# Kernel optimization log

Hardware: AMD Instinct MI355X
Metric: run time of the kernel (lower is better)

## Reference

```python
import jax, jax.numpy as jnp
import numpy as np

T, B, IN, H, L = 512, 128, 1024, 1024, 4
SCALE = 0.02  # scale randn-init weights so tanh/sigmoid stay in a sane range


def setup_inputs() -> dict:
    key = jax.random.key(0)
    ks = jax.random.split(key, 12)
    f32 = jnp.float32
    return {
        "x": jax.random.normal(ks[0], (T, B, IN), f32),
        "hidden": jax.random.normal(ks[1], (2 * L, B, H), f32) * 0.1,
        "Wii": jax.random.normal(ks[2], (L, 3 * H, IN), f32) * SCALE,
        "Wic": jax.random.normal(ks[3], (L, 3 * H, H), f32) * SCALE,
        "Wih": jax.random.normal(ks[4], (L, 3 * H, H), f32) * SCALE,
        "bii": jax.random.normal(ks[5], (L, 3 * H), f32) * SCALE,
        "bic": jax.random.normal(ks[6], (L, 3 * H), f32) * SCALE,
        "bih": jax.random.normal(ks[7], (L, 3 * H), f32) * SCALE,
        "Whh": jax.random.normal(ks[8], (L, H, H), f32) * SCALE,
        "bhh": jax.random.normal(ks[9], (L, H), f32) * SCALE,
        "Wir": jax.random.normal(ks[10], (L, H, IN), f32) * SCALE,
    }


def _res_lstm_scan(x, hidden, Wii, Wic, Wih, bii, bic, bih, Whh, bhh, Wir):
    n_layers = Wii.shape[0]
    h0, c0 = jnp.split(hidden, 2, axis=0)  # each [L, B, H]

    def step(carry, xt):
        h, c = carry
        out = xt
        new_h, new_c = [], []
        for j in range(n_layers):
            hj, cj = h[j], c[j]
            gates = (out @ Wii[j].T + bii[j]
                     + hj @ Wih[j].T + bih[j]
                     + cj @ Wic[j].T + bic[j])  # [B, 3H]
            i_g, f_g, o_g = jnp.split(gates, 3, axis=1)
            cellgate = jnp.tanh(hj @ Whh[j].T + bhh[j])
            cy = jax.nn.sigmoid(f_g) * cj + jax.nn.sigmoid(i_g) * cellgate
            hy = jax.nn.sigmoid(o_g) * (jnp.tanh(cy) + out @ Wir[j].T)
            out = hy
            new_h.append(hy)
            new_c.append(cy)
        return (jnp.stack(new_h), jnp.stack(new_c)), out

    (hF, cF), outputs = jax.lax.scan(step, (h0, c0), x)
    return outputs, hF, cF


def reference(x, hidden, Wii, Wic, Wih, bii, bic, bih, Whh, bhh, Wir):
    return _res_lstm_scan(x, hidden, Wii, Wic, Wih, bii, bic, bih, Whh, bhh, Wir)
```

## Files before the change

### kernel.cpp

```cpp
#include <hip/hip_runtime.h>


#define TT 512
#define BB 128
#define IN_D 1024
#define HH 1024
#define LL 4
#define G3 3072
#define NSUPER (TT + LL - 1)
#define KC 64
#define NCHUNK 48
#define SB_TILE 2048
#define SB_BUF 8192
#define SLOT (BB * HH)
#define SLOT_ALL (LL * SLOT)

typedef __attribute__((ext_vector_type(8))) __bf16 bf16x8;
typedef __attribute__((ext_vector_type(4))) __bf16 bf16x4;
typedef __attribute__((ext_vector_type(4))) float f32x4;

typedef __attribute__((address_space(3))) void lds_void;
typedef const __attribute__((address_space(1))) void gmem_void;

__device__ __forceinline__ void gload_lds16(const void* g, void* l) {
    __builtin_amdgcn_global_load_lds((gmem_void*)g, (lds_void*)l, 16, 0, 0);
}

__device__ __forceinline__ f32x4 mfma16(bf16x8 a, bf16x8 b, f32x4 c) {
    return __builtin_amdgcn_mfma_f32_16x16x32_bf16(a, b, c, 0, 0, 0);
}

__device__ __forceinline__ bf16x8 ldb(const __bf16* p, int k) {
    return *reinterpret_cast<const bf16x8*>(p + k);
}

__device__ __forceinline__ bf16x8 load_a(const float* p, int k) {
    float4 a0 = *reinterpret_cast<const float4*>(p + k);
    float4 a1 = *reinterpret_cast<const float4*>(p + k + 4);
    bf16x8 r;
    r[0] = (__bf16)a0.x; r[1] = (__bf16)a0.y; r[2] = (__bf16)a0.z; r[3] = (__bf16)a0.w;
    r[4] = (__bf16)a1.x; r[5] = (__bf16)a1.y; r[6] = (__bf16)a1.z; r[7] = (__bf16)a1.w;
    return r;
}

__device__ __forceinline__ float sigm(float v) { return 1.f / (1.f + __expf(-v)); }
__device__ __forceinline__ float tanh_fast(float v) { return 1.f - 2.f / (1.f + __expf(2.f * v)); }

__global__ void k_conv_gates(const float* __restrict__ Wii,
                             const float* __restrict__ Wic,
                             const float* __restrict__ Wih,
                             __bf16* __restrict__ Wg) {
    const unsigned total = (unsigned)LL * G3 * G3;
    const unsigned stride = gridDim.x * blockDim.x * 4u;
    for (unsigned idx = (blockIdx.x * blockDim.x + threadIdx.x) * 4u; idx < total; idx += stride) {
        unsigned row = idx / G3;
        int k = (int)(idx - row * G3);
        const float* src; int ks;
        if (k < 1024)      { src = Wii; ks = k; }
        else if (k < 2048) { src = Wih; ks = k - 1024; }
        else               { src = Wic; ks = k - 2048; }
        float4 v = *reinterpret_cast<const float4*>(src + (size_t)row * 1024 + ks);
        bf16x4 o;
        o[0] = (__bf16)v.x; o[1] = (__bf16)v.y; o[2] = (__bf16)v.z; o[3] = (__bf16)v.w;
        *reinterpret_cast<bf16x4*>(Wg + idx) = o;
    }
}

__global__ void k_conv_plain(const float* __restrict__ s, __bf16* __restrict__ d, unsigned total) {
    const unsigned stride = gridDim.x * blockDim.x * 4u;
    for (unsigned idx = (blockIdx.x * blockDim.x + threadIdx.x) * 4u; idx < total; idx += stride) {
        float4 v = *reinterpret_cast<const float4*>(s + idx);
        bf16x4 o;
        o[0] = (__bf16)v.x; o[1] = (__bf16)v.y; o[2] = (__bf16)v.z; o[3] = (__bf16)v.w;
        *reinterpret_cast<bf16x4*>(d + idx) = o;
    }
}

__global__ void k_bias(const float* __restrict__ bii, const float* __restrict__ bic,
                       const float* __restrict__ bih, const float* __restrict__ bhh,
                       float* __restrict__ bsum) {
    int i = blockIdx.x * blockDim.x + threadIdx.x;
    int j = i >> 12, n = i & 4095;
    if (j >= LL) return;
    if (n < G3) bsum[j * 4096 + n] = bii[j * G3 + n] + bih[j * G3 + n] + bic[j * G3 + n];
    else        bsum[j * 4096 + n] = bhh[j * HH + (n - G3)];
}

__global__ void k_init(const float* __restrict__ hidden,
                       float* __restrict__ cbufF, __bf16* __restrict__ hb, __bf16* __restrict__ cb) {
    const unsigned stride = gridDim.x * blockDim.x;
    for (unsigned i = blockIdx.x * blockDim.x + threadIdx.x; i < SLOT_ALL; i += stride) {
        float hv = hidden[i];
        float cv = hidden[SLOT_ALL + i];
        hb[SLOT_ALL + i] = (__bf16)hv;
        cb[SLOT_ALL + i] = (__bf16)cv;
        cbufF[SLOT_ALL + i] = cv;
    }
}

__global__ void k_final(const float* __restrict__ hfin, const float* __restrict__ cbufF,
                        float* __restrict__ out_tail) {
    const unsigned stride = gridDim.x * blockDim.x;
    for (unsigned i = blockIdx.x * blockDim.x + threadIdx.x; i < SLOT_ALL; i += stride) {
        out_tail[i] = hfin[i];
        out_tail[SLOT_ALL + i] = cbufF[SLOT_ALL + i];
    }
}

__global__ __launch_bounds__(512) void k_super(
    const float* __restrict__ x,
    const __bf16* __restrict__ Wg,
    const __bf16* __restrict__ Whh,
    const __bf16* __restrict__ Wir,
    const float* __restrict__ bsum,
    float* __restrict__ cbufF,
    __bf16* __restrict__ hb,
    __bf16* __restrict__ cb,
    float* __restrict__ hfin,
    float* __restrict__ dout,
    int s)
{
    const int j = blockIdx.y;
    const int t = s - j;
    if (t < 0 || t >= TT) return;

    __shared__ __align__(16) char smem[3 * SB_BUF];

    const int p = t & 1, pp = p ^ 1;
    const float*  csrcF = cbufF + (size_t)pp * SLOT_ALL + (size_t)j * SLOT;
    float*        cdstF = cbufF + (size_t)p  * SLOT_ALL + (size_t)j * SLOT;
    const __bf16* hsrcB = hb + (size_t)pp * SLOT_ALL + (size_t)j * SLOT;
    const __bf16* csrcB = cb + (size_t)pp * SLOT_ALL + (size_t)j * SLOT;
    const __bf16* osrcB = hb + (size_t)p * SLOT_ALL + (size_t)(j - 1) * SLOT;
    const float*  osrcF = x + (size_t)t * SLOT;
    __bf16* hdstB = hb + (size_t)p * SLOT_ALL + (size_t)j * SLOT;
    __bf16* cdstB = cb + (size_t)p * SLOT_ALL + (size_t)j * SLOT;

    const int tid  = threadIdx.x;
    const int lane = tid & 63;
    const int wave = tid >> 6;
    const int lrow = lane & 15;
    const int kgrp = lane >> 4;
    const int n0 = blockIdx.x * 16;
    const int m0 = wave * 16;

    const int st_tile = wave >> 1;
    const int st_half = wave & 1;
    const int st_r = st_half * 8 + (lane >> 3);
    const int st_s = lane & 7;
    const int st_k8 = ((st_s ^ (st_r & 7)) << 3);
    const __bf16* Wgj = Wg + (size_t)j * G3 * G3;
    const __bf16* st_g  = Wgj + (size_t)(st_tile * 1024 + n0 + st_r) * G3 + st_k8;
    const __bf16* st_wr = Wir + (size_t)j * HH * IN_D + (size_t)(n0 + st_r) * IN_D + st_k8;
    const __bf16* st_wc = Whh + (size_t)j * HH * HH + (size_t)(n0 + st_r) * HH + st_k8;
    char* st_dst = smem + st_tile * SB_TILE + st_half * 1024;

    auto stage = [&](int c) {
        if (c >= NCHUNK) return;
        char* dst = st_dst + (c % 3) * SB_BUF;
        if (st_tile < 3) {
            gload_lds16(st_g + (size_t)c * KC, dst);
        } else {
            const int r = c >> 4, kb = (c & 15) << 6;
            if (r == 0)      gload_lds16(st_wr + kb, dst);
            else if (r == 1) gload_lds16(st_wc + kb, dst);
        }
    };

    const int dsrow = lrow << 7;
    const int x7 = lrow & 7;
    const int so0 = ((kgrp ^ x7) << 4);
    const int so1 = (((4 | kgrp) ^ x7) << 4);

    const int aoff = (m0 + lrow) * HH + (kgrp << 3);
    const __bf16* aH = hsrcB + aoff;
    const __bf16* aC = csrcB + aoff;
    const __bf16* aO = osrcB + aoff;
    const float*  aX = osrcF + aoff;

    auto loadA = [&](int c, bf16x8& r0, bf16x8& r1) {
        const int rg = c >> 4, kt = (c & 15) << 6;
        if (rg == 0) {
            if (j == 0) { r0 = load_a(aX, kt); r1 = load_a(aX, kt + 32); }
            else        { r0 = ldb(aO, kt);    r1 = ldb(aO, kt + 32); }
        } else if (rg == 1) { r0 = ldb(aH, kt); r1 = ldb(aH, kt + 32); }
        else                { r0 = ldb(aC, kt); r1 = ldb(aC, kt + 32); }
    };

    f32x4 vi = {0,0,0,0}, vf = {0,0,0,0}, vo = {0,0,0,0}, vc = {0,0,0,0}, vr = {0,0,0,0};

    bf16x8 a0, a1, na0, na1;
    stage(0); stage(1);
    loadA(0, a0, a1);
    asm volatile("s_waitcnt vmcnt(3)" ::: "memory");
    __builtin_amdgcn_s_barrier();

    for (int c = 0; c < NCHUNK; ++c) {
        const int rg = c >> 4;
        char* bs = smem + (c % 3) * SB_BUF;

        if (c + 1 < NCHUNK) loadA(c + 1, na0, na1);
        stage(c + 2);

        bf16x8 b;
        b = *(const bf16x8*)(bs + 0 * SB_TILE + dsrow + so0); vi = mfma16(a0, b, vi);
        b = *(const bf16x8*)(bs + 1 * SB_TILE + dsrow + so0); vf = mfma16(a0, b, vf);
        b = *(const bf16x8*)(bs + 2 * SB_TILE + dsrow + so0); vo = mfma16(a0, b, vo);
        if (rg == 0)      { b = *(const bf16x8*)(bs + 3 * SB_TILE + dsrow + so0); vr = mfma16(a0, b, vr); }
        else if (rg == 1) { b = *(const bf16x8*)(bs + 3 * SB_TILE + dsrow + so0); vc = mfma16(a0, b, vc); }
        b = *(const bf16x8*)(bs + 0 * SB_TILE + dsrow + so1); vi = mfma16(a1, b, vi);
        b = *(const bf16x8*)(bs + 1 * SB_TILE + dsrow + so1); vf = mfma16(a1, b, vf);
        b = *(const bf16x8*)(bs + 2 * SB_TILE + dsrow + so1); vo = mfma16(a1, b, vo);
        if (rg == 0)      { b = *(const bf16x8*)(bs + 3 * SB_TILE + dsrow + so1); vr = mfma16(a1, b, vr); }
        else if (rg == 1) { b = *(const bf16x8*)(bs + 3 * SB_TILE + dsrow + so1); vc = mfma16(a1, b, vc); }

        a0 = na0; a1 = na1;
        asm volatile("s_waitcnt vmcnt(3)" ::: "memory");
        __builtin_amdgcn_s_barrier();
    }

    const int col = n0 + lrow;
    const float b_i = bsum[j * 4096 + col];
    const float b_f = bsum[j * 4096 + HH + col];
    const float b_o = bsum[j * 4096 + 2 * HH + col];
    const float b_c = bsum[j * 4096 + G3 + col];

    #pragma unroll
    for (int r = 0; r < 4; ++r) {
        const int m = m0 + kgrp * 4 + r;
        const size_t o = (size_t)m * HH + col;
        float iv = vi[r] + b_i;
        float fv = vf[r] + b_f;
        float ov = vo[r] + b_o;
        float cg = tanh_fast(vc[r] + b_c);
        float cold = csrcF[o];
        float cy = sigm(fv) * cold + sigm(iv) * cg;
        float hy = sigm(ov) * (tanh_fast(cy) + vr[r]);
        cdstF[o] = cy;
        cdstB[o] = (__bf16)cy;
        hdstB[o] = (__bf16)hy;
        if (t == TT - 1) hfin[(size_t)j * SLOT + o] = hy;
        if (j == LL - 1) dout[(size_t)t * SLOT + o] = hy;
    }
}

extern "C" void kernel_launch(void* const* d_in, const int* in_sizes, int n_in,
                              void* d_out, int out_size, void* d_ws, size_t ws_size,
                              hipStream_t stream) {
    const float* x      = (const float*)d_in[0];
    const float* hidden = (const float*)d_in[1];
    const float* Wii    = (const float*)d_in[2];
    const float* Wic    = (const float*)d_in[3];
    const float* Wih    = (const float*)d_in[4];
    const float* bii    = (const float*)d_in[5];
    const float* bic    = (const float*)d_in[6];
    const float* bih    = (const float*)d_in[7];
    const float* Whh    = (const float*)d_in[8];
    const float* bhh    = (const float*)d_in[9];
    const float* Wir    = (const float*)d_in[10];
    float* out = (float*)d_out;

    char* ws = (char*)d_ws;
    __bf16* Wg    = (__bf16*)(ws);
    __bf16* Whh_b = (__bf16*)(ws + 75497472);
    __bf16* Wir_b = (__bf16*)(ws + 83886080);
    float*  cbufF = (float*)(ws + 92274688);
    float*  bsum  = (float*)(ws + 96468992);
    __bf16* hb    = (__bf16*)(ws + 96534528);
    __bf16* cb    = (__bf16*)(ws + 98631680);
    float*  hfin  = (float*)(ws + 100728832);

    k_conv_gates<<<4096, 256, 0, stream>>>(Wii, Wic, Wih, Wg);
    k_conv_plain<<<2048, 256, 0, stream>>>(Whh, Whh_b, (unsigned)(LL * HH * HH));
    k_conv_plain<<<2048, 256, 0, stream>>>(Wir, Wir_b, (unsigned)(LL * HH * IN_D));
    k_bias<<<64, 256, 0, stream>>>(bii, bic, bih, bhh, bsum);
    k_init<<<1024, 256, 0, stream>>>(hidden, cbufF, hb, cb);

    dim3 grid(64, 4), block(512);
    for (int s = 0; s < NSUPER; ++s)
        k_super<<<grid, block, 0, stream>>>(x, Wg, Whh_b, Wir_b, bsum,
                                            cbufF, hb, cb, hfin, out, s);

    k_final<<<1024, 256, 0, stream>>>(hfin, cbufF, out + (size_t)TT * SLOT);
}
```

Baseline: 36.08 ms.

## Replace per-superstep kernel launches with a persistent kernel and grid barrier

The 515 per-superstep launches of k_super are replaced by one persistent kernel of 256 workgroups that loops over supersteps and synchronises through a global atomic counter barrier. This removes per-launch overhead and the gaps between launches on the serial wavefront schedule. The LDS weight staging ring also grows from three to four buffers, with a prefetch depth of three chunks. The design depends on all 256 workgroups being co-resident, since otherwise the spin barrier deadlocks. Weights are still streamed from global memory on every step.

```diff
diff --git a/kernel.cpp b/kernel.cpp
--- a/kernel.cpp
+++ b/kernel.cpp
@@ -12,8 +12,10 @@
 #define NCHUNK 48
 #define SB_TILE 2048
 #define SB_BUF 8192
+#define NBUF 4
 #define SLOT (BB * HH)
 #define SLOT_ALL (LL * SLOT)
+#define NWG 256
 
 typedef __attribute__((ext_vector_type(8))) __bf16 bf16x8;
 typedef __attribute__((ext_vector_type(4))) __bf16 bf16x4;
@@ -107,7 +109,7 @@
     }
 }
 
-__global__ __launch_bounds__(512) void k_super(
+__global__ __launch_bounds__(512, 2) void k_persist(
     const float* __restrict__ x,
     const __bf16* __restrict__ Wg,
     const __bf16* __restrict__ Whh,
@@ -118,24 +120,11 @@
     __bf16* __restrict__ cb,
     float* __restrict__ hfin,
     float* __restrict__ dout,
-    int s)
+    unsigned* __restrict__ bar)
 {
+    __shared__ __align__(16) char smem[NBUF * SB_BUF];
+
     const int j = blockIdx.y;
-    const int t = s - j;
-    if (t < 0 || t >= TT) return;
-
-    __shared__ __align__(16) char smem[3 * SB_BUF];
-
-    const int p = t & 1, pp = p ^ 1;
-    const float*  csrcF = cbufF + (size_t)pp * SLOT_ALL + (size_t)j * SLOT;
-    float*        cdstF = cbufF + (size_t)p  * SLOT_ALL + (size_t)j * SLOT;
-    const __bf16* hsrcB = hb + (size_t)pp * SLOT_ALL + (size_t)j * SLOT;
-    const __bf16* csrcB = cb + (size_t)pp * SLOT_ALL + (size_t)j * SLOT;
-    const __bf16* osrcB = hb + (size_t)p * SLOT_ALL + (size_t)(j - 1) * SLOT;
-    const float*  osrcF = x + (size_t)t * SLOT;
-    __bf16* hdstB = hb + (size_t)p * SLOT_ALL + (size_t)j * SLOT;
-    __bf16* cdstB = cb + (size_t)p * SLOT_ALL + (size_t)j * SLOT;
-
     const int tid  = threadIdx.x;
     const int lane = tid & 63;
     const int wave = tid >> 6;
@@ -155,92 +144,112 @@
     const __bf16* st_wc = Whh + (size_t)j * HH * HH + (size_t)(n0 + st_r) * HH + st_k8;
     char* st_dst = smem + st_tile * SB_TILE + st_half * 1024;
 
-    auto stage = [&](int c) {
-        if (c >= NCHUNK) return;
-        char* dst = st_dst + (c % 3) * SB_BUF;
-        if (st_tile < 3) {
-            gload_lds16(st_g + (size_t)c * KC, dst);
-        } else {
-            const int r = c >> 4, kb = (c & 15) << 6;
-            if (r == 0)      gload_lds16(st_wr + kb, dst);
-            else if (r == 1) gload_lds16(st_wc + kb, dst);
-        }
-    };
-
     const int dsrow = lrow << 7;
     const int x7 = lrow & 7;
     const int so0 = ((kgrp ^ x7) << 4);
     const int so1 = (((4 | kgrp) ^ x7) << 4);
-
     const int aoff = (m0 + lrow) * HH + (kgrp << 3);
-    const __bf16* aH = hsrcB + aoff;
-    const __bf16* aC = csrcB + aoff;
-    const __bf16* aO = osrcB + aoff;
-    const float*  aX = osrcF + aoff;
-
-    auto loadA = [&](int c, bf16x8& r0, bf16x8& r1) {
-        const int rg = c >> 4, kt = (c & 15) << 6;
-        if (rg == 0) {
-            if (j == 0) { r0 = load_a(aX, kt); r1 = load_a(aX, kt + 32); }
-            else        { r0 = ldb(aO, kt);    r1 = ldb(aO, kt + 32); }
-        } else if (rg == 1) { r0 = ldb(aH, kt); r1 = ldb(aH, kt + 32); }
-        else                { r0 = ldb(aC, kt); r1 = ldb(aC, kt + 32); }
-    };
-
-    f32x4 vi = {0,0,0,0}, vf = {0,0,0,0}, vo = {0,0,0,0}, vc = {0,0,0,0}, vr = {0,0,0,0};
-
-    bf16x8 a0, a1, na0, na1;
-    stage(0); stage(1);
-    loadA(0, a0, a1);
-    asm volatile("s_waitcnt vmcnt(3)" ::: "memory");
-    __builtin_amdgcn_s_barrier();
-
-    for (int c = 0; c < NCHUNK; ++c) {
-        const int rg = c >> 4;
-        char* bs = smem + (c % 3) * SB_BUF;
-
-        if (c + 1 < NCHUNK) loadA(c + 1, na0, na1);
-        stage(c + 2);
-
-        bf16x8 b;
-        b = *(const bf16x8*)(bs + 0 * SB_TILE + dsrow + so0); vi = mfma16(a0, b, vi);
-        b = *(const bf16x8*)(bs + 1 * SB_TILE + dsrow + so0); vf = mfma16(a0, b, vf);
-        b = *(const bf16x8*)(bs + 2 * SB_TILE + dsrow + so0); vo = mfma16(a0, b, vo);
-        if (rg == 0)      { b = *(const bf16x8*)(bs + 3 * SB_TILE + dsrow + so0); vr = mfma16(a0, b, vr); }
-        else if (rg == 1) { b = *(const bf16x8*)(bs + 3 * SB_TILE + dsrow + so0); vc = mfma16(a0, b, vc); }
-        b = *(const bf16x8*)(bs + 0 * SB_TILE + dsrow + so1); vi = mfma16(a1, b, vi);
-        b = *(const bf16x8*)(bs + 1 * SB_TILE + dsrow + so1); vf = mfma16(a1, b, vf);
-        b = *(const bf16x8*)(bs + 2 * SB_TILE + dsrow + so1); vo = mfma16(a1, b, vo);
-        if (rg == 0)      { b = *(const bf16x8*)(bs + 3 * SB_TILE + dsrow + so1); vr = mfma16(a1, b, vr); }
-        else if (rg == 1) { b = *(const bf16x8*)(bs + 3 * SB_TILE + dsrow + so1); vc = mfma16(a1, b, vc); }
-
-        a0 = na0; a1 = na1;
-        asm volatile("s_waitcnt vmcnt(3)" ::: "memory");
-        __builtin_amdgcn_s_barrier();
-    }
-
     const int col = n0 + lrow;
+
     const float b_i = bsum[j * 4096 + col];
     const float b_f = bsum[j * 4096 + HH + col];
     const float b_o = bsum[j * 4096 + 2 * HH + col];
     const float b_c = bsum[j * 4096 + G3 + col];
 
-    #pragma unroll
-    for (int r = 0; r < 4; ++r) {
-        const int m = m0 + kgrp * 4 + r;
-        const size_t o = (size_t)m * HH + col;
-        float iv = vi[r] + b_i;
-        float fv = vf[r] + b_f;
-        float ov = vo[r] + b_o;
-        float cg = tanh_fast(vc[r] + b_c);
-        float cold = csrcF[o];
-        float cy = sigm(fv) * cold + sigm(iv) * cg;
-        float hy = sigm(ov) * (tanh_fast(cy) + vr[r]);
-        cdstF[o] = cy;
-        cdstB[o] = (__bf16)cy;
-        hdstB[o] = (__bf16)hy;
-        if (t == TT - 1) hfin[(size_t)j * SLOT + o] = hy;
-        if (j == LL - 1) dout[(size_t)t * SLOT + o] = hy;
+    for (int s = 0; s < NSUPER; ++s) {
+        const int t = s - j;
+        if (t >= 0 && t < TT) {
+            const int p = t & 1, pp = p ^ 1;
+            const float*  csrcF = cbufF + (size_t)pp * SLOT_ALL + (size_t)j * SLOT;
+            float*        cdstF = cbufF + (size_t)p  * SLOT_ALL + (size_t)j * SLOT;
+            const __bf16* aH = hb + (size_t)pp * SLOT_ALL + (size_t)j * SLOT + aoff;
+            const __bf16* aC = cb + (size_t)pp * SLOT_ALL + (size_t)j * SLOT + aoff;
+            const __bf16* aO = hb + (size_t)p * SLOT_ALL + (size_t)(j - 1) * SLOT + aoff;
+            const float*  aX = x + (size_t)t * SLOT + aoff;
+            __bf16* hdstB = hb + (size_t)p * SLOT_ALL + (size_t)j * SLOT;
+            __bf16* cdstB = cb + (size_t)p * SLOT_ALL + (size_t)j * SLOT;
+
+            auto stage = [&](int c) {
+                if (c >= NCHUNK) return;
+                char* dst = st_dst + (c % NBUF) * SB_BUF;
+                if (st_tile < 3) {
+                    gload_lds16(st_g + (size_t)c * KC, dst);
+                } else {
+                    const int r = c >> 4, kb = (c & 15) << 6;
+                    if (r == 0)      gload_lds16(st_wr + kb, dst);
+                    else if (r == 1) gload_lds16(st_wc + kb, dst);
+                }
+            };
+            auto loadA = [&](int c, bf16x8& r0, bf16x8& r1) {
+                const int rg = c >> 4, kt = (c & 15) << 6;
+                if (rg == 0) {
+                    if (j == 0) { r0 = load_a(aX, kt); r1 = load_a(aX, kt + 32); }
+                    else        { r0 = ldb(aO, kt);    r1 = ldb(aO, kt + 32); }
+                } else if (rg == 1) { r0 = ldb(aH, kt); r1 = ldb(aH, kt + 32); }
+                else                { r0 = ldb(aC, kt); r1 = ldb(aC, kt + 32); }
+            };
+
+            f32x4 vi = {0,0,0,0}, vf = {0,0,0,0}, vo = {0,0,0,0}, vc = {0,0,0,0}, vr = {0,0,0,0};
+            bf16x8 a0, a1, na0, na1;
+
+            stage(0); stage(1); stage(2);
+            loadA(0, a0, a1);
+            asm volatile("s_waitcnt vmcnt(4)" ::: "memory");
+            __builtin_amdgcn_s_barrier();
+
+            for (int c = 0; c < NCHUNK; ++c) {
+                const int rg = c >> 4;
+                char* bs = smem + (c % NBUF) * SB_BUF;
+
+                if (c + 1 < NCHUNK) loadA(c + 1, na0, na1);
+                stage(c + 3);
+
+                bf16x8 b;
+                b = *(const bf16x8*)(bs + 0 * SB_TILE + dsrow + so0); vi = mfma16(a0, b, vi);
+                b = *(const bf16x8*)(bs + 1 * SB_TILE + dsrow + so0); vf = mfma16(a0, b, vf);
+                b = *(const bf16x8*)(bs + 2 * SB_TILE + dsrow + so0); vo = mfma16(a0, b, vo);
+                if (rg == 0)      { b = *(const bf16x8*)(bs + 3 * SB_TILE + dsrow + so0); vr = mfma16(a0, b, vr); }
+                else if (rg == 1) { b = *(const bf16x8*)(bs + 3 * SB_TILE + dsrow + so0); vc = mfma16(a0, b, vc); }
+                b = *(const bf16x8*)(bs + 0 * SB_TILE + dsrow + so1); vi = mfma16(a1, b, vi);
+                b = *(const bf16x8*)(bs + 1 * SB_TILE + dsrow + so1); vf = mfma16(a1, b, vf);
+                b = *(const bf16x8*)(bs + 2 * SB_TILE + dsrow + so1); vo = mfma16(a1, b, vo);
+                if (rg == 0)      { b = *(const bf16x8*)(bs + 3 * SB_TILE + dsrow + so1); vr = mfma16(a1, b, vr); }
+                else if (rg == 1) { b = *(const bf16x8*)(bs + 3 * SB_TILE + dsrow + so1); vc = mfma16(a1, b, vc); }
+
+                a0 = na0; a1 = na1;
+                asm volatile("s_waitcnt vmcnt(4)" ::: "memory");
+                __builtin_amdgcn_s_barrier();
+            }
+
+            #pragma unroll
+            for (int r = 0; r < 4; ++r) {
+                const int m = m0 + kgrp * 4 + r;
+                const size_t o = (size_t)m * HH + col;
+                float iv = vi[r] + b_i;
+                float fv = vf[r] + b_f;
+                float ov = vo[r] + b_o;
+                float cg = tanh_fast(vc[r] + b_c);
+                float cold = csrcF[o];
+                float cy = sigm(fv) * cold + sigm(iv) * cg;
+                float hy = sigm(ov) * (tanh_fast(cy) + vr[r]);
+                cdstF[o] = cy;
+                cdstB[o] = (__bf16)cy;
+                hdstB[o] = (__bf16)hy;
+                if (t == TT - 1) hfin[(size_t)j * SLOT + o] = hy;
+                if (j == LL - 1) dout[(size_t)t * SLOT + o] = hy;
+            }
+        }
+
+        __syncthreads();
+        if (tid == 0) {
+            __threadfence();
+            __hip_atomic_fetch_add(bar, 1u, __ATOMIC_RELAXED, __HIP_MEMORY_SCOPE_AGENT);
+            const unsigned tgt = (unsigned)(s + 1) * NWG;
+            while (__hip_atomic_load(bar, __ATOMIC_ACQUIRE, __HIP_MEMORY_SCOPE_AGENT) < tgt)
+                __builtin_amdgcn_s_sleep(2);
+            __threadfence();
+        }
+        __syncthreads();
     }
 }
 
@@ -269,17 +278,18 @@
     __bf16* hb    = (__bf16*)(ws + 96534528);
     __bf16* cb    = (__bf16*)(ws + 98631680);
     float*  hfin  = (float*)(ws + 100728832);
-
+    unsigned* bar = (unsigned*)(ws + 102825984);
+
+    hipMemsetAsync(bar, 0, 64, stream);
     k_conv_gates<<<4096, 256, 0, stream>>>(Wii, Wic, Wih, Wg);
     k_conv_plain<<<2048, 256, 0, stream>>>(Whh, Whh_b, (unsigned)(LL * HH * HH));
     k_conv_plain<<<2048, 256, 0, stream>>>(Wir, Wir_b, (unsigned)(LL * HH * IN_D));
     k_bias<<<64, 256, 0, stream>>>(bii, bic, bih, bhh, bsum);
     k_init<<<1024, 256, 0, stream>>>(hidden, cbufF, hb, cb);
 
-    dim3 grid(64, 4), block(512);
-    for (int s = 0; s < NSUPER; ++s)
-        k_super<<<grid, block, 0, stream>>>(x, Wg, Whh_b, Wir_b, bsum,
-                                            cbufF, hb, cb, hfin, out, s);
+    dim3 grid(64, LL), block(512);
+    k_persist<<<grid, block, 0, stream>>>(x, Wg, Whh_b, Wir_b, bsum,
+                                          cbufF, hb, cb, hfin, out, bar);
 
     k_final<<<1024, 256, 0, stream>>>(hfin, cbufF, out + (size_t)TT * SLOT);
 }
```

After: 55.86 ms. +54.8%, slower.

## Stage activation panels through LDS with 4-deep async pipeline and smaller K chunks

Applied to the files above, without the earlier changes.

The A operand (previous layer output, h, c) is no longer loaded directly from global memory into registers by each wave. Waves 4-7 now stage it into LDS with async global-to-LDS loads, alongside the weight tiles loaded by waves 0-3. The K chunk is halved to 32 and the ring buffer deepened to 4 stages with a 3-chunk lookahead, aiming to hide global latency better. The cost is twice as many barriers per step, and layer 0 still converts x from fp32 in registers.

```diff
diff --git a/kernel.cpp b/kernel.cpp
--- a/kernel.cpp
+++ b/kernel.cpp
@@ -8,10 +8,12 @@
 #define LL 4
 #define G3 3072
 #define NSUPER (TT + LL - 1)
-#define KC 64
-#define NCHUNK 48
-#define SB_TILE 2048
-#define SB_BUF 8192
+#define KC 32
+#define NCHUNK 96
+#define B_AREA 4096
+#define A_AREA 8192
+#define BUF_SZ (B_AREA + A_AREA)
+#define NBUF 4
 #define SLOT (BB * HH)
 #define SLOT_ALL (LL * SLOT)
 
@@ -30,16 +32,12 @@
     return __builtin_amdgcn_mfma_f32_16x16x32_bf16(a, b, c, 0, 0, 0);
 }
 
-__device__ __forceinline__ bf16x8 ldb(const __bf16* p, int k) {
-    return *reinterpret_cast<const bf16x8*>(p + k);
-}
-
-__device__ __forceinline__ bf16x8 load_a(const float* p, int k) {
-    float4 a0 = *reinterpret_cast<const float4*>(p + k);
-    float4 a1 = *reinterpret_cast<const float4*>(p + k + 4);
+__device__ __forceinline__ int srow(int r) { return (r & 3) ^ ((r >> 2) & 3); }
+
+__device__ __forceinline__ bf16x8 cvt8(float4 u, float4 v) {
     bf16x8 r;
-    r[0] = (__bf16)a0.x; r[1] = (__bf16)a0.y; r[2] = (__bf16)a0.z; r[3] = (__bf16)a0.w;
-    r[4] = (__bf16)a1.x; r[5] = (__bf16)a1.y; r[6] = (__bf16)a1.z; r[7] = (__bf16)a1.w;
+    r[0] = (__bf16)u.x; r[1] = (__bf16)u.y; r[2] = (__bf16)u.z; r[3] = (__bf16)u.w;
+    r[4] = (__bf16)v.x; r[5] = (__bf16)v.y; r[6] = (__bf16)v.z; r[7] = (__bf16)v.w;
     return r;
 }
 
@@ -124,15 +122,14 @@
     const int t = s - j;
     if (t < 0 || t >= TT) return;
 
-    __shared__ __align__(16) char smem[3 * SB_BUF];
+    __shared__ __align__(16) char smem[NBUF * BUF_SZ];
 
     const int p = t & 1, pp = p ^ 1;
     const float*  csrcF = cbufF + (size_t)pp * SLOT_ALL + (size_t)j * SLOT;
     float*        cdstF = cbufF + (size_t)p  * SLOT_ALL + (size_t)j * SLOT;
-    const __bf16* hsrcB = hb + (size_t)pp * SLOT_ALL + (size_t)j * SLOT;
-    const __bf16* csrcB = cb + (size_t)pp * SLOT_ALL + (size_t)j * SLOT;
-    const __bf16* osrcB = hb + (size_t)p * SLOT_ALL + (size_t)(j - 1) * SLOT;
-    const float*  osrcF = x + (size_t)t * SLOT;
+    const __bf16* panH = hb + (size_t)pp * SLOT_ALL + (size_t)j * SLOT;
+    const __bf16* panC = cb + (size_t)pp * SLOT_ALL + (size_t)j * SLOT;
+    const __bf16* panO = hb + (size_t)p * SLOT_ALL + (size_t)(j - 1) * SLOT;
     __bf16* hdstB = hb + (size_t)p * SLOT_ALL + (size_t)j * SLOT;
     __bf16* cdstB = cb + (size_t)p * SLOT_ALL + (size_t)j * SLOT;
 
@@ -144,78 +141,96 @@
     const int n0 = blockIdx.x * 16;
     const int m0 = wave * 16;
 
-    const int st_tile = wave >> 1;
-    const int st_half = wave & 1;
-    const int st_r = st_half * 8 + (lane >> 3);
-    const int st_s = lane & 7;
-    const int st_k8 = ((st_s ^ (st_r & 7)) << 3);
+    const int bs_row = lane >> 2;
+    const int bs_phys = lane & 3;
+    const int bs_k8 = ((bs_phys ^ srow(bs_row)) << 3);
     const __bf16* Wgj = Wg + (size_t)j * G3 * G3;
-    const __bf16* st_g  = Wgj + (size_t)(st_tile * 1024 + n0 + st_r) * G3 + st_k8;
-    const __bf16* st_wr = Wir + (size_t)j * HH * IN_D + (size_t)(n0 + st_r) * IN_D + st_k8;
-    const __bf16* st_wc = Whh + (size_t)j * HH * HH + (size_t)(n0 + st_r) * HH + st_k8;
-    char* st_dst = smem + st_tile * SB_TILE + st_half * 1024;
+    const __bf16* st_g  = Wgj + (size_t)(wave * 1024 + n0 + bs_row) * G3 + bs_k8;
+    const __bf16* st_wr = Wir + (size_t)j * HH * IN_D + (size_t)(n0 + bs_row) * IN_D + bs_k8;
+    const __bf16* st_wc = Whh + (size_t)j * HH * HH + (size_t)(n0 + bs_row) * HH + bs_k8;
+    const int bs_dst = wave * 1024 + lane * 16;
+
+    const int ao = (wave - 4) * 2;
+    const int as_rowin = lane >> 2;
+    const int as_phys = lane & 3;
+    const int as_k8 = ((as_phys ^ srow(as_rowin)) << 3);
+    const int as_row0 = ao * 16 + as_rowin;
+    const size_t paoff0 = (size_t)as_row0 * HH + as_k8;
+    const size_t paoff1 = paoff0 + (size_t)16 * HH;
+    const int as_dst0 = B_AREA + ao * 1024 + lane * 16;
+    const int as_dst1 = as_dst0 + 1024;
+
+    const int bswz = ((kgrp ^ srow(lrow)) << 4);
+    const int boff0 = 0 * 1024 + lrow * 64 + bswz;
+    const int boff1 = 1 * 1024 + lrow * 64 + bswz;
+    const int boff2 = 2 * 1024 + lrow * 64 + bswz;
+    const int boff3 = 3 * 1024 + lrow * 64 + bswz;
+    const int aoff = B_AREA + (m0 + lrow) * 64 + bswz;
+
+    const float* aX = x + (size_t)t * SLOT + (size_t)(m0 + lrow) * IN_D + kgrp * 8;
 
     auto stage = [&](int c) {
         if (c >= NCHUNK) return;
-        char* dst = st_dst + (c % 3) * SB_BUF;
-        if (st_tile < 3) {
-            gload_lds16(st_g + (size_t)c * KC, dst);
+        const int rg = c >> 5;
+        const int kk = (c & 31) << 5;
+        char* buf = smem + (c & 3) * BUF_SZ;
+        if (wave < 3) {
+            gload_lds16(st_g + rg * 1024 + kk, buf + bs_dst);
+        } else if (wave == 3) {
+            if (rg == 0)      gload_lds16(st_wr + kk, buf + bs_dst);
+            else              gload_lds16(st_wc + kk, buf + bs_dst);
         } else {
-            const int r = c >> 4, kb = (c & 15) << 6;
-            if (r == 0)      gload_lds16(st_wr + kb, dst);
-            else if (r == 1) gload_lds16(st_wc + kb, dst);
+            if (rg == 0) {
+                if (j > 0) {
+                    gload_lds16(panO + paoff0 + kk, buf + as_dst0);
+                    gload_lds16(panO + paoff1 + kk, buf + as_dst1);
+                }
+            } else if (rg == 1) {
+                gload_lds16(panH + paoff0 + kk, buf + as_dst0);
+                gload_lds16(panH + paoff1 + kk, buf + as_dst1);
+            } else {
+                gload_lds16(panC + paoff0 + kk, buf + as_dst0);
+                gload_lds16(panC + paoff1 + kk, buf + as_dst1);
+            }
         }
     };
 
-    const int dsrow = lrow << 7;
-    const int x7 = lrow & 7;
-    const int so0 = ((kgrp ^ x7) << 4);
-    const int so1 = (((4 | kgrp) ^ x7) << 4);
-
-    const int aoff = (m0 + lrow) * HH + (kgrp << 3);
-    const __bf16* aH = hsrcB + aoff;
-    const __bf16* aC = csrcB + aoff;
-    const __bf16* aO = osrcB + aoff;
-    const float*  aX = osrcF + aoff;
-
-    auto loadA = [&](int c, bf16x8& r0, bf16x8& r1) {
-        const int rg = c >> 4, kt = (c & 15) << 6;
-        if (rg == 0) {
-            if (j == 0) { r0 = load_a(aX, kt); r1 = load_a(aX, kt + 32); }
-            else        { r0 = ldb(aO, kt);    r1 = ldb(aO, kt + 32); }
-        } else if (rg == 1) { r0 = ldb(aH, kt); r1 = ldb(aH, kt + 32); }
-        else                { r0 = ldb(aC, kt); r1 = ldb(aC, kt + 32); }
-    };
-
     f32x4 vi = {0,0,0,0}, vf = {0,0,0,0}, vo = {0,0,0,0}, vc = {0,0,0,0}, vr = {0,0,0,0};
 
-    bf16x8 a0, a1, na0, na1;
-    stage(0); stage(1);
-    loadA(0, a0, a1);
-    asm volatile("s_waitcnt vmcnt(3)" ::: "memory");
+    float4 x0, x1;
+    if (j == 0) { x0 = *(const float4*)(aX); x1 = *(const float4*)(aX + 4); }
+
+    stage(0); stage(1); stage(2);
+    if (wave < 4) asm volatile("s_waitcnt vmcnt(2)" ::: "memory");
+    else          asm volatile("s_waitcnt vmcnt(4)" ::: "memory");
     __builtin_amdgcn_s_barrier();
 
     for (int c = 0; c < NCHUNK; ++c) {
-        const int rg = c >> 4;
-        char* bs = smem + (c % 3) * SB_BUF;
-
-        if (c + 1 < NCHUNK) loadA(c + 1, na0, na1);
-        stage(c + 2);
+        const int rg = c >> 5;
+        char* buf = smem + (c & 3) * BUF_SZ;
+
+        bf16x8 a;
+        if (j == 0 && rg == 0) {
+            a = cvt8(x0, x1);
+            if (c + 1 < 32) {
+                const float* px = aX + ((c + 1) << 5);
+                x0 = *(const float4*)(px); x1 = *(const float4*)(px + 4);
+            }
+        } else {
+            a = *(const bf16x8*)(buf + aoff);
+        }
+
+        stage(c + 3);
 
         bf16x8 b;
-        b = *(const bf16x8*)(bs + 0 * SB_TILE + dsrow + so0); vi = mfma16(a0, b, vi);
-        b = *(const bf16x8*)(bs + 1 * SB_TILE + dsrow + so0); vf = mfma16(a0, b, vf);
-        b = *(const bf16x8*)(bs + 2 * SB_TILE + dsrow + so0); vo = mfma16(a0, b, vo);
-        if (rg == 0)      { b = *(const bf16x8*)(bs + 3 * SB_TILE + dsrow + so0); vr = mfma16(a0, b, vr); }
-        else if (rg == 1) { b = *(const bf16x8*)(bs + 3 * SB_TILE + dsrow + so0); vc = mfma16(a0, b, vc); }
-        b = *(const bf16x8*)(bs + 0 * SB_TILE + dsrow + so1); vi = mfma16(a1, b, vi);
-        b = *(const bf16x8*)(bs + 1 * SB_TILE + dsrow + so1); vf = mfma16(a1, b, vf);
-        b = *(const bf16x8*)(bs + 2 * SB_TILE + dsrow + so1); vo = mfma16(a1, b, vo);
-        if (rg == 0)      { b = *(const bf16x8*)(bs + 3 * SB_TILE + dsrow + so1); vr = mfma16(a1, b, vr); }
-        else if (rg == 1) { b = *(const bf16x8*)(bs + 3 * SB_TILE + dsrow + so1); vc = mfma16(a1, b, vc); }
-
-        a0 = na0; a1 = na1;
-        asm volatile("s_waitcnt vmcnt(3)" ::: "memory");
+        b = *(const bf16x8*)(buf + boff0); vi = mfma16(a, b, vi);
+        b = *(const bf16x8*)(buf + boff1); vf = mfma16(a, b, vf);
+        b = *(const bf16x8*)(buf + boff2); vo = mfma16(a, b, vo);
+        if (rg == 0)      { b = *(const bf16x8*)(buf + boff3); vr = mfma16(a, b, vr); }
+        else if (rg == 1) { b = *(const bf16x8*)(buf + boff3); vc = mfma16(a, b, vc); }
+
+        if (wave < 4) asm volatile("s_waitcnt vmcnt(2)" ::: "memory");
+        else          asm volatile("s_waitcnt vmcnt(4)" ::: "memory");
         __builtin_amdgcn_s_barrier();
     }
 
@@ -276,7 +291,7 @@
     k_bias<<<64, 256, 0, stream>>>(bii, bic, bih, bhh, bsum);
     k_init<<<1024, 256, 0, stream>>>(hidden, cbufF, hb, cb);
 
-    dim3 grid(64, 4), block(512);
+    dim3 grid(64, LL), block(512);
     for (int s = 0; s < NSUPER; ++s)
         k_super<<<grid, block, 0, stream>>>(x, Wg, Whh_b, Wir_b, bsum,
                                             cbufF, hb, cb, hfin, out, s);
```

Measured after the change: 36.18 ms. Within noise of the previous version (+0.3%).
